# Kernel tuning notes

Measured on AMD Instinct MI355X. Metric: run time of the kernel, lower is better.

## Reference

```python
import jax, jax.numpy as jnp
import numpy as np

D_IN = 1024
D_OUT = 1024
N_HEADS = 16
D_K = D_OUT // N_HEADS
ROPE_THETA = 10000.0


def setup_inputs() -> dict:
    key = jax.random.key(0)
    ks = jax.random.split(key, 5)
    x = jax.random.normal(ks[0], (2, 2048, D_IN), dtype=jnp.float32)
    token_positions = jnp.arange(2048, dtype=jnp.int32)
    scale = 0.02
    wq = jax.random.normal(ks[1], (D_OUT, D_IN), dtype=jnp.float32) * scale
    wk = jax.random.normal(ks[2], (D_OUT, D_IN), dtype=jnp.float32) * scale
    wv = jax.random.normal(ks[3], (D_OUT, D_IN), dtype=jnp.float32) * scale
    wo = jax.random.normal(ks[4], (D_OUT, D_OUT), dtype=jnp.float32) * scale
    return {"x": x, "token_positions": token_positions, "wq": wq, "wk": wk, "wv": wv, "wo": wo}


def _rope(x, token_positions):
    # x: [..., S, d_k]; token_positions: [S]
    d_k = x.shape[-1]
    idx = jnp.arange(d_k)
    k = idx // 2
    # thetas[i, j] = pos_i / theta^(2*(j//2)/d_k)
    angles = token_positions[:, None].astype(x.dtype) / jnp.power(
        jnp.asarray(ROPE_THETA, x.dtype), 2.0 * k.astype(x.dtype) / d_k
    )  # [S, d_k]
    cos = jnp.cos(angles)
    sin = jnp.sin(angles) * jnp.where(idx % 2 == 0, -1.0, 1.0).astype(x.dtype)
    pair_swaps = idx + jnp.where(idx % 2 == 0, 1, -1)  # swap even/odd pairs
    return x * cos + x[..., pair_swaps] * sin


def _forward(x, token_positions, wq, wk, wv, wo):
    B, S, _ = x.shape
    # fused QKV projection (same math as concat + split)
    q = jnp.einsum("bsd,od->bso", x, wq)
    k = jnp.einsum("bsd,od->bso", x, wk)
    v = jnp.einsum("bsd,od->bso", x, wv)
    # split heads: [B, S, H*dk] -> [B, H, S, dk]
    split = lambda t: t.reshape(B, S, N_HEADS, D_K).transpose(0, 2, 1, 3)
    q, k, v = split(q), split(k), split(v)
    q = _rope(q, token_positions)
    k = _rope(k, token_positions)
    scores = jnp.einsum("bhqd,bhkd->bhqk", q, k) / jnp.sqrt(jnp.asarray(D_K, x.dtype))
    causal = jnp.tril(jnp.ones((S, S), dtype=bool))
    scores = jnp.where(causal, scores, -jnp.inf)
    probs = jax.nn.softmax(scores, axis=-1)
    ctx = jnp.einsum("bhqk,bhkd->bhqd", probs, v)
    merged = ctx.transpose(0, 2, 1, 3).reshape(B, S, D_OUT)
    return jnp.einsum("bsm,om->bso", merged, wo)


def reference(x, token_positions, wq, wk, wv, wo):
    return _forward(x, token_positions, wq, wk, wv, wo)
```

## Files before the change

kernel.cpp:

```cpp
#include <hip/hip_runtime.h>

#define D_MODEL 1024
#define SEQ     2048
#define BATCH   2
#define NHEADS  16
#define DK      64
#define NROWS   (BATCH*SEQ)

typedef unsigned short u16;
typedef __bf16 bf16x8 __attribute__((ext_vector_type(8)));
typedef float  f32x4  __attribute__((ext_vector_type(4)));

__device__ __forceinline__ u16 f2bf(float f) {
    union { float f; unsigned u; } v; v.f = f;
    unsigned u = v.u;
    u += 0x7fffu + ((u >> 16) & 1);
    return (u16)(u >> 16);
}
__device__ __forceinline__ float bf2f(u16 h) {
    union { unsigned u; float f; } v; v.u = ((unsigned)h) << 16;
    return v.f;
}
__device__ __forceinline__ unsigned cvtpk_bf16(float lo, float hi) {
    unsigned r;
    asm("v_cvt_pk_bf16_f32 %0, %1, %2" : "=v"(r) : "v"(lo), "v"(hi));
    return r;
}

__device__ __forceinline__ void gload_lds16(const u16* g, u16* l) {
    __builtin_amdgcn_global_load_lds(
        (const __attribute__((address_space(1))) void*)g,
        (__attribute__((address_space(3))) void*)l, 16, 0, 0);
}

__global__ void cvt_bf16_all(const float* __restrict__ x,
                             const float* __restrict__ w0, const float* __restrict__ w1,
                             const float* __restrict__ w2, const float* __restrict__ w3,
                             u16* __restrict__ xb, u16* __restrict__ wb) {
    int i = blockIdx.x * blockDim.x + threadIdx.x;
    int row = i >> 8;
    int c   = (i & 255) * 4;
    const float* src; u16* dst;
    if (row < 4096) {
        src = x + (size_t)row * 1024;
        dst = xb + (size_t)row * 1024;
    } else {
        int r2 = row - 4096;
        int ws = r2 >> 10;
        int rr = r2 & 1023;
        const float* wsrc = ws == 0 ? w0 : ws == 1 ? w1 : ws == 2 ? w2 : w3;
        src = wsrc + (size_t)rr * 1024;
        dst = wb + ((size_t)ws << 20) + (size_t)rr * 1024;
    }
    float4 v = *(const float4*)(src + c);
    uint2 o;
    o.x = (unsigned)f2bf(v.x) | ((unsigned)f2bf(v.y) << 16);
    o.y = (unsigned)f2bf(v.z) | ((unsigned)f2bf(v.w) << 16);
    *(uint2*)(dst + c) = o;
}

__global__ __launch_bounds__(256) void gemm_qkv_p(
    const u16* __restrict__ A, const u16* __restrict__ W,
    u16* __restrict__ Qp, u16* __restrict__ Kp, u16* __restrict__ Vt)
{
    __shared__ __align__(16) u16 Ash[128 * 32];
    __shared__ __align__(16) u16 Bsh[128 * 32];

    const int m0  = blockIdx.x * 128;
    const int sel = blockIdx.y >> 3;
    const int n0  = (blockIdx.y & 7) * 128;
    const u16* B = W + ((size_t)sel << 20);
    const int tid = threadIdx.x;
    const int lane = tid & 63;
    const int w    = tid >> 6;
    const int wr = w >> 1, wc = w & 1;
    const int fr = lane & 15;
    const int fk = (lane >> 4) * 8;
    const int rsub = lane >> 2;
    const int csub = (lane & 3) * 8;

    f32x4 acc[4][4];
#pragma unroll
    for (int i = 0; i < 4; ++i)
#pragma unroll
        for (int j = 0; j < 4; ++j) acc[i][j] = (f32x4){0.f, 0.f, 0.f, 0.f};

    for (int k0 = 0; k0 < 1024; k0 += 32) {
        __syncthreads();
        const u16* Ab = A + (size_t)(m0 + 16 * w + rsub) * 1024 + k0 + csub;
        const u16* Bb = B + (size_t)(n0 + 16 * w + rsub) * 1024 + k0 + csub;
#pragma unroll
        for (int half = 0; half < 2; ++half) {
            size_t ro = (size_t)(half * 64) * 1024;
            int lo = (half * 64 + 16 * w) * 32;
            gload_lds16(Ab + ro, &Ash[lo]);
            gload_lds16(Bb + ro, &Bsh[lo]);
        }
        __syncthreads();

        bf16x8 ah[4], bh[4];
#pragma unroll
        for (int i = 0; i < 4; ++i)
            ah[i] = *(const bf16x8*)&Ash[(wr * 64 + i * 16 + fr) * 32 + fk];
#pragma unroll
        for (int j = 0; j < 4; ++j)
            bh[j] = *(const bf16x8*)&Bsh[(wc * 64 + j * 16 + fr) * 32 + fk];
#pragma unroll
        for (int i = 0; i < 4; ++i)
#pragma unroll
            for (int j = 0; j < 4; ++j)
                acc[i][j] = __builtin_amdgcn_mfma_f32_16x16x32_bf16(ah[i], bh[j], acc[i][j], 0, 0, 0);
    }

    const int r0 = (lane >> 4) * 4;
#pragma unroll
    for (int i = 0; i < 4; ++i) {
#pragma unroll
        for (int j = 0; j < 4; ++j) {
            int col = n0 + wc * 64 + j * 16 + fr;
#pragma unroll
            for (int r = 0; r < 4; ++r) {
                int row = m0 + wr * 64 + i * 16 + r0 + r;
                u16 v = f2bf(acc[i][j][r]);
                if (sel == 0)      Qp[(size_t)row * 1024 + col] = v;
                else if (sel == 1) Kp[(size_t)row * 1024 + col] = v;
                else               Vt[(size_t)col * NROWS + row] = v;
            }
        }
    }
}

__global__ __launch_bounds__(256) void gemm_out_p(
    const u16* __restrict__ A, const u16* __restrict__ B, float* __restrict__ Cout)
{
    __shared__ __align__(16) u16 Ash[128 * 32];
    __shared__ __align__(16) u16 Bsh[128 * 32];

    const int m0 = blockIdx.x * 128;
    const int n0 = blockIdx.y * 128;
    const int tid = threadIdx.x;
    const int lane = tid & 63;
    const int w    = tid >> 6;
    const int wr = w >> 1, wc = w & 1;
    const int fr = lane & 15;
    const int fk = (lane >> 4) * 8;
    const int rsub = lane >> 2;
    const int csub = (lane & 3) * 8;

    f32x4 acc[4][4];
#pragma unroll
    for (int i = 0; i < 4; ++i)
#pragma unroll
        for (int j = 0; j < 4; ++j) acc[i][j] = (f32x4){0.f, 0.f, 0.f, 0.f};

    for (int k0 = 0; k0 < 1024; k0 += 32) {
        __syncthreads();
        const u16* Ab = A + (size_t)(m0 + 16 * w + rsub) * 1024 + k0 + csub;
        const u16* Bb = B + (size_t)(n0 + 16 * w + rsub) * 1024 + k0 + csub;
#pragma unroll
        for (int half = 0; half < 2; ++half) {
            size_t ro = (size_t)(half * 64) * 1024;
            int lo = (half * 64 + 16 * w) * 32;
            gload_lds16(Ab + ro, &Ash[lo]);
            gload_lds16(Bb + ro, &Bsh[lo]);
        }
        __syncthreads();

        bf16x8 ah[4], bh[4];
#pragma unroll
        for (int i = 0; i < 4; ++i)
            ah[i] = *(const bf16x8*)&Ash[(wr * 64 + i * 16 + fr) * 32 + fk];
#pragma unroll
        for (int j = 0; j < 4; ++j)
            bh[j] = *(const bf16x8*)&Bsh[(wc * 64 + j * 16 + fr) * 32 + fk];
#pragma unroll
        for (int i = 0; i < 4; ++i)
#pragma unroll
            for (int j = 0; j < 4; ++j)
                acc[i][j] = __builtin_amdgcn_mfma_f32_16x16x32_bf16(ah[i], bh[j], acc[i][j], 0, 0, 0);
    }

    const int r0 = (lane >> 4) * 4;
#pragma unroll
    for (int i = 0; i < 4; ++i) {
#pragma unroll
        for (int j = 0; j < 4; ++j) {
            int col = n0 + wc * 64 + j * 16 + fr;
#pragma unroll
            for (int r = 0; r < 4; ++r)
                Cout[(size_t)(m0 + wr * 64 + i * 16 + r0 + r) * 1024 + col] = acc[i][j][r];
        }
    }
}

__global__ void rope_plain(u16* __restrict__ qk, const int* __restrict__ pos) {
    int i = blockIdx.x * blockDim.x + threadIdx.x;
    int p = i & 511;
    int n = i >> 9;
    int s = n & 2047;
    int k = p & 31;
    int h = p >> 5;
    size_t base = (size_t)n * 1024 + h * DK + 2 * k;
    unsigned v = *(const unsigned*)&qk[base];
    float x0 = bf2f((u16)(v & 0xffff));
    float x1 = bf2f((u16)(v >> 16));
    float ang = (float)pos[s] * expf((float)k * -0.28782313662425575f);
    float c = cosf(ang), sn = sinf(ang);
    float qs = (n < 4096) ? 0.18033688011112042f : 1.0f;
    c *= qs; sn *= qs;
    float y0 = x0 * c - x1 * sn;
    float y1 = x1 * c + x0 * sn;
    *(unsigned*)&qk[base] = (unsigned)f2bf(y0) | ((unsigned)f2bf(y1) << 16);
}

__global__ __launch_bounds__(512, 4) void attn_v7(
    const u16* __restrict__ Qp, const u16* __restrict__ Kp, const u16* __restrict__ Vt,
    u16* __restrict__ Op, float* __restrict__ mlbuf)
{
    const int slot = 39 - (int)blockIdx.x;
    const int h = blockIdx.y, b = blockIdx.z;
    int g, rr;
    if (slot < 4)       { g = 0; rr = slot; }
    else if (slot < 12) { g = 1; rr = slot - 4; }
    else if (slot < 24) { g = 2; rr = slot - 12; }
    else                { g = 3; rr = slot - 24; }
    const int qq  = rr / (g + 1);
    const int qt2 = 4 * g + qq;
    const int c   = rr - qq * (g + 1);

    const int tid  = threadIdx.x;
    const int lane = tid & 63;
    const int w    = tid >> 6;
    const int fr = lane & 15;
    const int fg = lane >> 4;
    const int bS = b * SEQ;
    const int hd = h * DK;
    const int qbase = qt2 * 128 + 16 * w;
    const int ntk = 2 * qt2 + 2;
    const int kt0 = 8 * c;
    const int kt1 = min(8 * c + 8, ntk);

    __shared__ __align__(16) u16 Kl[2][64 * 64];
    __shared__ __align__(16) u16 Vl[2][64 * 64];
    __shared__ __align__(16) u16 Plds[8][16][72];

    const int srow = 8 * w + (lane >> 3);
    const int scol = (((lane & 7) ^ (lane >> 3)) * 8);
    const int swz  = (fr & 7) * 8;

    const u16* qrow = Qp + (size_t)(bS + qbase + fr) * 1024 + hd;
    bf16x8 qf0 = *(const bf16x8*)(qrow + fg * 8);
    bf16x8 qf1 = *(const bf16x8*)(qrow + 32 + fg * 8);

    f32x4 o[4];
#pragma unroll
    for (int j = 0; j < 4; ++j) o[j] = (f32x4){0.f, 0.f, 0.f, 0.f};
    float mrow = -1e30f, lrow = 0.f;

#define STAGE(BUF, KT) do { \
    int kb_ = (KT) * 64; \
    gload_lds16(Kp + (size_t)(bS + kb_ + srow) * 1024 + hd + scol, &Kl[BUF][(8 * w) * 64]); \
    gload_lds16(Vt + (size_t)(hd + srow) * NROWS + bS + kb_ + scol, &Vl[BUF][(8 * w) * 64]); \
} while (0)

    STAGE(0, kt0);
    __syncthreads();

    int cur = 0;
    for (int kt = kt0; kt < kt1; ++kt) {
        if (kt + 1 < kt1) STAGE(cur ^ 1, kt + 1);
        const int k0 = kt * 64;
        if (k0 <= qbase + 15) {
            bf16x8 kf[4][2];
#pragma unroll
            for (int t = 0; t < 4; ++t) {
                const u16* kr = &Kl[cur][(16 * t + fr) * 64];
                kf[t][0] = *(const bf16x8*)(kr + ((fg * 8) ^ swz));
                kf[t][1] = *(const bf16x8*)(kr + (((4 + fg) * 8) ^ swz));
            }
            f32x4 sc4[4];
#pragma unroll
            for (int t = 0; t < 4; ++t) {
                f32x4 a = (f32x4){0.f, 0.f, 0.f, 0.f};
                a = __builtin_amdgcn_mfma_f32_16x16x32_bf16(kf[t][0], qf0, a, 0, 0, 0);
                a = __builtin_amdgcn_mfma_f32_16x16x32_bf16(kf[t][1], qf1, a, 0, 0, 0);
                sc4[t] = a;
            }
            float p[4][4];
#pragma unroll
            for (int t = 0; t < 4; ++t)
#pragma unroll
                for (int r = 0; r < 4; ++r) p[t][r] = sc4[t][r];
            if (k0 + 63 > qbase) {
#pragma unroll
                for (int t = 0; t < 4; ++t)
#pragma unroll
                    for (int r = 0; r < 4; ++r)
                        if (k0 + 16 * t + 4 * fg + r > qbase + fr) p[t][r] = -1e30f;
            }
            float a0 = fmaxf(fmaxf(p[0][0], p[0][1]), fmaxf(p[0][2], p[0][3]));
            float a1 = fmaxf(fmaxf(p[1][0], p[1][1]), fmaxf(p[1][2], p[1][3]));
            float a2 = fmaxf(fmaxf(p[2][0], p[2][1]), fmaxf(p[2][2], p[2][3]));
            float a3 = fmaxf(fmaxf(p[3][0], p[3][1]), fmaxf(p[3][2], p[3][3]));
            float mx = fmaxf(fmaxf(a0, a1), fmaxf(a2, a3));
            mx = fmaxf(mx, __shfl_xor(mx, 16));
            mx = fmaxf(mx, __shfl_xor(mx, 32));
            float scf = 1.0f;
            if (!__all(mx <= mrow + 8.0f)) {
                float mnew = fmaxf(mrow, mx);
                scf = exp2f(mrow - mnew);
                float s0 = __shfl(scf, 4 * fg);
                float s1 = __shfl(scf, 4 * fg + 1);
                float s2 = __shfl(scf, 4 * fg + 2);
                float s3 = __shfl(scf, 4 * fg + 3);
#pragma unroll
                for (int j = 0; j < 4; ++j) {
                    o[j][0] *= s0; o[j][1] *= s1; o[j][2] *= s2; o[j][3] *= s3;
                }
                mrow = mnew;
            }
            float rs = 0.f;
#pragma unroll
            for (int t = 0; t < 4; ++t)
#pragma unroll
                for (int r = 0; r < 4; ++r) {
                    p[t][r] = exp2f(p[t][r] - mrow);
                    rs += p[t][r];
                }
            rs += __shfl_xor(rs, 16);
            rs += __shfl_xor(rs, 32);
            lrow = lrow * scf + rs;
#pragma unroll
            for (int t = 0; t < 4; ++t) {
                uint2 pk;
                pk.x = cvtpk_bf16(p[t][0], p[t][1]);
                pk.y = cvtpk_bf16(p[t][2], p[t][3]);
                *(uint2*)&Plds[w][fr][16 * t + 4 * fg] = pk;
            }
            bf16x8 pf0 = *(const bf16x8*)&Plds[w][fr][fg * 8];
            bf16x8 pf1 = *(const bf16x8*)&Plds[w][fr][32 + fg * 8];
#pragma unroll
            for (int j = 0; j < 4; ++j) {
                const u16* vr = &Vl[cur][(16 * j + fr) * 64];
                bf16x8 v0 = *(const bf16x8*)(vr + ((fg * 8) ^ swz));
                bf16x8 v1 = *(const bf16x8*)(vr + (((4 + fg) * 8) ^ swz));
                o[j] = __builtin_amdgcn_mfma_f32_16x16x32_bf16(pf0, v0, o[j], 0, 0, 0);
                o[j] = __builtin_amdgcn_mfma_f32_16x16x32_bf16(pf1, v1, o[j], 0, 0, 0);
            }
        }
        __syncthreads();
        cur ^= 1;
    }
#undef STAGE

    const int slotg = (b * NHEADS + h) * 40 + slot;
#pragma unroll
    for (int r = 0; r < 4; ++r) {
        int rrel = 16 * w + 4 * fg + r;
#pragma unroll
        for (int j = 0; j < 4; ++j)
            Op[((size_t)slotg * 128 + rrel) * 64 + 16 * j + fr] = f2bf(o[j][r]);
    }
    if (fg == 0) {
        float* pp = mlbuf + ((size_t)slotg * 128 + 16 * w + fr) * 2;
        pp[0] = mrow;
        pp[1] = lrow;
    }
}

__global__ void attn_combine3(const u16* __restrict__ Op, const float* __restrict__ mlbuf,
                              u16* __restrict__ Mb) {
    int i = blockIdx.x * blockDim.x + threadIdx.x;
    int row = i >> 7;
    int c8  = (i & 127) * 8;
    int h   = c8 >> 6;
    int s   = row & 2047;
    int b   = row >> 11;
    int qt2 = s >> 7;
    int g   = qt2 >> 2;
    int nch = g + 1;
    int slot0 = (b * NHEADS + h) * 40 + 2 * g * (g + 1) + (qt2 & 3) * (g + 1);
    int rrel = s & 127, crel = c8 & 63;

    float mv[4], lv[4];
    float m = -1e30f;
    for (int k = 0; k < nch; ++k) {
        const float* pp = mlbuf + ((size_t)(slot0 + k) * 128 + rrel) * 2;
        mv[k] = pp[0]; lv[k] = pp[1];
        m = fmaxf(m, mv[k]);
    }
    float L = 0.f;
    for (int k = 0; k < nch; ++k) {
        mv[k] = exp2f(mv[k] - m);
        L += lv[k] * mv[k];
    }
    float acc[8];
#pragma unroll
    for (int jj = 0; jj < 8; ++jj) acc[jj] = 0.f;
    for (int k = 0; k < nch; ++k) {
        float wgt = mv[k];
        uint4 u = *(const uint4*)(Op + ((size_t)(slot0 + k) * 128 + rrel) * 64 + crel);
        const unsigned* wrd = (const unsigned*)&u;
#pragma unroll
        for (int kk = 0; kk < 4; ++kk) {
            acc[2 * kk]     += wgt * bf2f((u16)(wrd[kk] & 0xffff));
            acc[2 * kk + 1] += wgt * bf2f((u16)(wrd[kk] >> 16));
        }
    }
    float inv = 1.0f / L;
    unsigned ou[4];
#pragma unroll
    for (int kk = 0; kk < 4; ++kk)
        ou[kk] = (unsigned)f2bf(acc[2 * kk] * inv) | ((unsigned)f2bf(acc[2 * kk + 1] * inv) << 16);
    *(uint4*)(Mb + (size_t)row * 1024 + c8) = *(uint4*)ou;
}

extern "C" void kernel_launch(void* const* d_in, const int* in_sizes, int n_in,
                              void* d_out, int out_size, void* d_ws, size_t ws_size,
                              hipStream_t stream) {
    const float* x   = (const float*)d_in[0];
    const int*   pos = (const int*)d_in[1];
    const float* wq  = (const float*)d_in[2];
    const float* wk  = (const float*)d_in[3];
    const float* wv  = (const float*)d_in[4];
    const float* wo  = (const float*)d_in[5];
    float* out = (float*)d_out;

    char* ws = (char*)d_ws;
    u16* xb  = (u16*)(ws);
    u16* wb  = (u16*)(ws + (24ull << 20));
    u16* wob = wb + 3 * (1 << 20);
    u16* Qp  = (u16*)(ws + (32ull << 20));
    u16* Kp  = (u16*)(ws + (40ull << 20));
    u16* Vt  = (u16*)(ws + (48ull << 20));
    u16* Mb  = (u16*)(ws + (56ull << 20));
    u16* Op  = (u16*)(ws);
    float* mlbuf = (float*)(ws + (21ull << 20));

    cvt_bf16_all<<<8192, 256, 0, stream>>>(x, wq, wk, wv, wo, xb, wb);

    gemm_qkv_p<<<dim3(NROWS / 128, 24), 256, 0, stream>>>(xb, wb, Qp, Kp, Vt);

    rope_plain<<<16384, 256, 0, stream>>>(Qp, pos);

    attn_v7<<<dim3(40, NHEADS, BATCH), 512, 0, stream>>>(Qp, Kp, Vt, Op, mlbuf);
    attn_combine3<<<2048, 256, 0, stream>>>(Op, mlbuf, Mb);

    gemm_out_p<<<dim3(NROWS / 128, 8), 256, 0, stream>>>(Mb, wob, out);
}
```

Baseline: 155.5 us.

## Fuse RoPE into QKV GEMM epilogue and restage attention K/V loads via registers

Applies RoPE and the Q scaling inside the QKV GEMM epilogue, using a lane shuffle to fetch the partner element, and removes the separate rope kernel along with its extra read/write pass over Q and K. The attention kernel now prefetches K/V tiles two steps ahead into registers and writes them to LDS with ordinary stores, replacing direct global-to-LDS loads. It also raises the launch-bounds occupancy hint from 4 to 6 and brackets the MFMA sections with s_setprio. The epilogue now computes sin/cos per element, and the register prefetch adds register pressure that may conflict with the higher occupancy target.

```diff
diff --git a/kernel.cpp b/kernel.cpp
--- a/kernel.cpp
+++ b/kernel.cpp
@@ -60,7 +60,7 @@
 }
 
 __global__ __launch_bounds__(256) void gemm_qkv_p(
-    const u16* __restrict__ A, const u16* __restrict__ W,
+    const u16* __restrict__ A, const u16* __restrict__ W, const int* __restrict__ pos,
     u16* __restrict__ Qp, u16* __restrict__ Kp, u16* __restrict__ Vt)
 {
     __shared__ __align__(16) u16 Ash[128 * 32];
@@ -113,18 +113,37 @@
     }
 
     const int r0 = (lane >> 4) * 4;
-#pragma unroll
-    for (int i = 0; i < 4; ++i) {
+    if (sel == 2) {
+#pragma unroll
+        for (int i = 0; i < 4; ++i)
+#pragma unroll
+            for (int j = 0; j < 4; ++j) {
+                int col = n0 + wc * 64 + j * 16 + fr;
+#pragma unroll
+                for (int r = 0; r < 4; ++r)
+                    Vt[(size_t)col * NROWS + (m0 + wr * 64 + i * 16 + r0 + r)] = f2bf(acc[i][j][r]);
+            }
+    } else {
+        const float qs  = (sel == 0) ? 0.18033688011112042f : 1.0f;
+        const float sgn = (fr & 1) ? 1.0f : -1.0f;
+        u16* Outp = (sel == 0) ? Qp : Kp;
 #pragma unroll
         for (int j = 0; j < 4; ++j) {
             int col = n0 + wc * 64 + j * 16 + fr;
-#pragma unroll
-            for (int r = 0; r < 4; ++r) {
-                int row = m0 + wr * 64 + i * 16 + r0 + r;
-                u16 v = f2bf(acc[i][j][r]);
-                if (sel == 0)      Qp[(size_t)row * 1024 + col] = v;
-                else if (sel == 1) Kp[(size_t)row * 1024 + col] = v;
-                else               Vt[(size_t)col * NROWS + row] = v;
+            int kpi = (j * 16 + fr) >> 1;
+            float ek = expf((float)kpi * -0.28782313662425575f);
+#pragma unroll
+            for (int i = 0; i < 4; ++i) {
+#pragma unroll
+                for (int r = 0; r < 4; ++r) {
+                    int row = m0 + wr * 64 + i * 16 + r0 + r;
+                    float ang = (float)pos[row & 2047] * ek;
+                    float c = cosf(ang), sn = sinf(ang);
+                    float v  = acc[i][j][r];
+                    float px = __shfl_xor(v, 1);
+                    float y  = (v * c + px * sn * sgn) * qs;
+                    Outp[(size_t)row * 1024 + col] = f2bf(y);
+                }
             }
         }
     }
@@ -193,27 +212,7 @@
     }
 }
 
-__global__ void rope_plain(u16* __restrict__ qk, const int* __restrict__ pos) {
-    int i = blockIdx.x * blockDim.x + threadIdx.x;
-    int p = i & 511;
-    int n = i >> 9;
-    int s = n & 2047;
-    int k = p & 31;
-    int h = p >> 5;
-    size_t base = (size_t)n * 1024 + h * DK + 2 * k;
-    unsigned v = *(const unsigned*)&qk[base];
-    float x0 = bf2f((u16)(v & 0xffff));
-    float x1 = bf2f((u16)(v >> 16));
-    float ang = (float)pos[s] * expf((float)k * -0.28782313662425575f);
-    float c = cosf(ang), sn = sinf(ang);
-    float qs = (n < 4096) ? 0.18033688011112042f : 1.0f;
-    c *= qs; sn *= qs;
-    float y0 = x0 * c - x1 * sn;
-    float y1 = x1 * c + x0 * sn;
-    *(unsigned*)&qk[base] = (unsigned)f2bf(y0) | ((unsigned)f2bf(y1) << 16);
-}
-
-__global__ __launch_bounds__(512, 4) void attn_v7(
+__global__ __launch_bounds__(512, 6) void attn_v8(
     const u16* __restrict__ Qp, const u16* __restrict__ Kp, const u16* __restrict__ Vt,
     u16* __restrict__ Op, float* __restrict__ mlbuf)
 {
@@ -244,9 +243,10 @@
     __shared__ __align__(16) u16 Vl[2][64 * 64];
     __shared__ __align__(16) u16 Plds[8][16][72];
 
-    const int srow = 8 * w + (lane >> 3);
-    const int scol = (((lane & 7) ^ (lane >> 3)) * 8);
-    const int swz  = (fr & 7) * 8;
+    const int dsrow  = 8 * w + (lane >> 3);
+    const int lincol = (lane & 7) * 8;
+    const int dsoff  = dsrow * 64 + (((lane & 7) ^ (lane >> 3)) * 8);
+    const int swz    = (fr & 7) * 8;
 
     const u16* qrow = Qp + (size_t)(bS + qbase + fr) * 1024 + hd;
     bf16x8 qf0 = *(const bf16x8*)(qrow + fg * 8);
@@ -257,18 +257,27 @@
     for (int j = 0; j < 4; ++j) o[j] = (f32x4){0.f, 0.f, 0.f, 0.f};
     float mrow = -1e30f, lrow = 0.f;
 
-#define STAGE(BUF, KT) do { \
-    int kb_ = (KT) * 64; \
-    gload_lds16(Kp + (size_t)(bS + kb_ + srow) * 1024 + hd + scol, &Kl[BUF][(8 * w) * 64]); \
-    gload_lds16(Vt + (size_t)(hd + srow) * NROWS + bS + kb_ + scol, &Vl[BUF][(8 * w) * 64]); \
+    uint4 kreg, vreg;
+#define LOADR(KT) do { \
+    kreg = *(const uint4*)(Kp + (size_t)(bS + (KT) * 64 + dsrow) * 1024 + hd + lincol); \
+    vreg = *(const uint4*)(Vt + (size_t)(hd + dsrow) * NROWS + bS + (KT) * 64 + lincol); \
 } while (0)
-
-    STAGE(0, kt0);
+#define DSW(BUF) do { \
+    *(uint4*)&Kl[BUF][dsoff] = kreg; \
+    *(uint4*)&Vl[BUF][dsoff] = vreg; \
+} while (0)
+
+    LOADR(kt0);
+    DSW(0);
+    if (kt0 + 1 < kt1) LOADR(kt0 + 1);
     __syncthreads();
 
     int cur = 0;
     for (int kt = kt0; kt < kt1; ++kt) {
-        if (kt + 1 < kt1) STAGE(cur ^ 1, kt + 1);
+        if (kt + 1 < kt1) {
+            DSW(cur ^ 1);
+            if (kt + 2 < kt1) LOADR(kt + 2);
+        }
         const int k0 = kt * 64;
         if (k0 <= qbase + 15) {
             bf16x8 kf[4][2];
@@ -279,6 +288,7 @@
                 kf[t][1] = *(const bf16x8*)(kr + (((4 + fg) * 8) ^ swz));
             }
             f32x4 sc4[4];
+            __builtin_amdgcn_s_setprio(1);
 #pragma unroll
             for (int t = 0; t < 4; ++t) {
                 f32x4 a = (f32x4){0.f, 0.f, 0.f, 0.f};
@@ -286,6 +296,7 @@
                 a = __builtin_amdgcn_mfma_f32_16x16x32_bf16(kf[t][1], qf1, a, 0, 0, 0);
                 sc4[t] = a;
             }
+            __builtin_amdgcn_s_setprio(0);
             float p[4][4];
 #pragma unroll
             for (int t = 0; t < 4; ++t)
@@ -339,6 +350,7 @@
             }
             bf16x8 pf0 = *(const bf16x8*)&Plds[w][fr][fg * 8];
             bf16x8 pf1 = *(const bf16x8*)&Plds[w][fr][32 + fg * 8];
+            __builtin_amdgcn_s_setprio(1);
 #pragma unroll
             for (int j = 0; j < 4; ++j) {
                 const u16* vr = &Vl[cur][(16 * j + fr) * 64];
@@ -347,11 +359,13 @@
                 o[j] = __builtin_amdgcn_mfma_f32_16x16x32_bf16(pf0, v0, o[j], 0, 0, 0);
                 o[j] = __builtin_amdgcn_mfma_f32_16x16x32_bf16(pf1, v1, o[j], 0, 0, 0);
             }
+            __builtin_amdgcn_s_setprio(0);
         }
         __syncthreads();
         cur ^= 1;
     }
-#undef STAGE
+#undef LOADR
+#undef DSW
 
     const int slotg = (b * NHEADS + h) * 40 + slot;
 #pragma unroll
@@ -439,11 +453,9 @@
 
     cvt_bf16_all<<<8192, 256, 0, stream>>>(x, wq, wk, wv, wo, xb, wb);
 
-    gemm_qkv_p<<<dim3(NROWS / 128, 24), 256, 0, stream>>>(xb, wb, Qp, Kp, Vt);
-
-    rope_plain<<<16384, 256, 0, stream>>>(Qp, pos);
-
-    attn_v7<<<dim3(40, NHEADS, BATCH), 512, 0, stream>>>(Qp, Kp, Vt, Op, mlbuf);
+    gemm_qkv_p<<<dim3(NROWS / 128, 24), 256, 0, stream>>>(xb, wb, pos, Qp, Kp, Vt);
+
+    attn_v8<<<dim3(40, NHEADS, BATCH), 512, 0, stream>>>(Qp, Kp, Vt, Op, mlbuf);
     attn_combine3<<<2048, 256, 0, stream>>>(Op, mlbuf, Mb);
 
     gemm_out_p<<<dim3(NROWS / 128, 8), 256, 0, stream>>>(Mb, wob, out);
```

Measured after the change: 533.8 us. 3.43x slower.
